# Kernel optimization log

Hardware: AMD Instinct MI355X
Metric: run time of the kernel (lower is better)

## Reference

```python
import jax, jax.numpy as jnp
import numpy as np

B, S, D, H, HD, R = 1, 3072, 2048, 16, 128, 16
ALPHA = 16.0
EPS = 1e-6


def _rope_freqs():
    # standard RoPE angles, interleave-duplicated so freqs[..., 0::2] gives the
    # per-pair cos values exactly as the torch module slices them
    inv = 1.0 / (10000.0 ** (np.arange(0, HD, 2, dtype=np.float32) / HD))  # [HD/2]
    ang = np.arange(S, dtype=np.float32)[:, None] * inv[None, :]           # [S, HD/2]
    cos = np.repeat(np.cos(ang), 2, axis=-1).reshape(1, S, 1, HD)
    sin = np.repeat(np.sin(ang), 2, axis=-1).reshape(1, S, 1, HD)
    return jnp.asarray(cos), jnp.asarray(sin)


def setup_inputs() -> dict:
    key = jax.random.key(0)
    ks = jax.random.split(key, 18)
    n = jax.random.normal
    WS = 0.02  # weight init scale
    freqs_cos, freqs_sin = _rope_freqs()
    return {
        "hidden_states": n(ks[0], (B, S, D), jnp.float32),
        "wq": n(ks[1], (D, D), jnp.float32) * WS,
        "bq": n(ks[2], (D,), jnp.float32) * WS,
        "wk": n(ks[3], (D, D), jnp.float32) * WS,
        "bk": n(ks[4], (D,), jnp.float32) * WS,
        "wv": n(ks[5], (D, D), jnp.float32) * WS,
        "bv": n(ks[6], (D,), jnp.float32) * WS,
        "wo": n(ks[7], (D, D), jnp.float32) * WS,
        "bo": n(ks[8], (D,), jnp.float32) * WS,
        "lq_down": n(ks[9], (R, D), jnp.float32) / R,
        "lq_up": n(ks[10], (D, R), jnp.float32) * WS,
        "lk_down": n(ks[11], (R, D), jnp.float32) / R,
        "lk_up": n(ks[12], (D, R), jnp.float32) * WS,
        "lv_down": n(ks[13], (R, D), jnp.float32) / R,
        "lv_up": n(ks[14], (D, R), jnp.float32) * WS,
        "lo_down": n(ks[15], (R, D), jnp.float32) / R,
        "lo_up": n(ks[16], (D, R), jnp.float32) * WS,
        "norm_q_w": jnp.ones((D,), jnp.float32),
        "norm_k_w": jnp.ones((D,), jnp.float32),
        "freqs_cos": freqs_cos,
        "freqs_sin": freqs_sin,
    }


def _lora(x, w_down, w_up, scale):
    return (x @ w_down.T) @ w_up.T * scale


def _rmsnorm(x, w):
    return x * jax.lax.rsqrt(jnp.mean(x * x, axis=-1, keepdims=True) + EPS) * w


def _apply_rotary(x, freqs_cos, freqs_sin):
    # x: [B,S,H,HD]; freqs: [1,S,1,HD]
    x1, x2 = x[..., 0::2], x[..., 1::2]
    c = freqs_cos[..., 0::2]
    s = freqs_sin[..., 1::2]
    even = x1 * c - x2 * s
    odd = x1 * s + x2 * c
    return jnp.stack([even, odd], axis=-1).reshape(x.shape)


def reference(hidden_states, wq, bq, wk, bk, wv, bv, wo, bo,
              lq_down, lq_up, lk_down, lk_up, lv_down, lv_up, lo_down, lo_up,
              norm_q_w, norm_k_w, freqs_cos, freqs_sin):
    scale = ALPHA / R
    x = hidden_states
    # qkv projections + LoRA adds (self-attention: encoder_hidden_states = hidden_states)
    q = x @ wq.T + bq + _lora(x, lq_down, lq_up, scale)
    k = x @ wk.T + bk + _lora(x, lk_down, lk_up, scale)
    v = x @ wv.T + bv + _lora(x, lv_down, lv_up, scale)
    # RMSNorm over full d_model, then split heads
    q = _rmsnorm(q, norm_q_w).reshape(B, S, H, HD)
    k = _rmsnorm(k, norm_k_w).reshape(B, S, H, HD)
    v = v.reshape(B, S, H, HD)
    # custom strided rotary embedding
    q = _apply_rotary(q, freqs_cos, freqs_sin)
    k = _apply_rotary(k, freqs_cos, freqs_sin)
    # SDPA (non-causal, no mask)
    scores = jnp.einsum('bihd,bjhd->bhij', q, k) / jnp.sqrt(jnp.float32(HD))
    attn = jax.nn.softmax(scores, axis=-1)
    o = jnp.einsum('bhij,bjhd->bihd', attn, v).reshape(B, S, D)
    # output projection + LoRA
    out = o @ wo.T + bo + _lora(o, lo_down, lo_up, scale)
    return out
```

## Files before the change

### kernel.cpp

```cpp
#include <hip/hip_runtime.h>
#include <stdint.h>

#define S_LEN 3072
#define DIM   2048
#define NH    16
#define HDIM  128
#define RANK  16
#define EPS_F 1e-6f
#define LORA_SCALE 1.0f
#define QK_SCALE 0.08838834764831845f
#define SM_MAX 24.0f

typedef unsigned short u16;
typedef __attribute__((ext_vector_type(8))) short short8;
typedef __attribute__((ext_vector_type(4))) float f32x4;
typedef __attribute__((ext_vector_type(16))) float f32x16;
typedef __attribute__((ext_vector_type(4))) unsigned short u16x4;
typedef __attribute__((ext_vector_type(8))) unsigned short u16x8;
typedef __attribute__((ext_vector_type(2))) unsigned short u16x2;
typedef __attribute__((ext_vector_type(4))) float float4a;
typedef __attribute__((ext_vector_type(4))) unsigned int uint4a;

__device__ __forceinline__ u16 f2b(float f) {
  uint32_t u = __builtin_bit_cast(uint32_t, f);
  u += 0x7fffu + ((u >> 16) & 1u);
  return (u16)(u >> 16);
}
__device__ __forceinline__ float b2f(u16 b) {
  uint32_t u = ((uint32_t)b) << 16;
  return __builtin_bit_cast(float, u);
}

__device__ __forceinline__ unsigned cvt_pk_bf16(float lo, float hi) {
  unsigned r;
  asm("v_cvt_pk_bf16_f32 %0, %1, %2" : "=v"(r) : "v"(lo), "v"(hi));
  return r;
}
__device__ __forceinline__ void pl32_swap(unsigned& a, unsigned& b) {
  asm("v_permlane32_swap_b32 %0, %1" : "+v"(a), "+v"(b));
}

__device__ __forceinline__ void g2l16(const void* g, void* l) {
  __builtin_amdgcn_global_load_lds(
      (__attribute__((address_space(1))) unsigned int*)g,
      (__attribute__((address_space(3))) unsigned int*)l, 16, 0, 0);
}

__global__ __launch_bounds__(256) void convf2b(const float* __restrict__ in,
                                               u16* __restrict__ out) {
  int i = (blockIdx.x * 256 + threadIdx.x) * 4;
  float4a v = *(const float4a*)(in + i);
  u16x4 o = { f2b(v[0]), f2b(v[1]), f2b(v[2]), f2b(v[3]) };
  *(u16x4*)(out + i) = o;
}

__global__ __launch_bounds__(256) void fold_lora4(
    const float* __restrict__ w0, const float* __restrict__ w1,
    const float* __restrict__ w2, const float* __restrict__ w3,
    const float* __restrict__ u0, const float* __restrict__ u1,
    const float* __restrict__ u2, const float* __restrict__ u3,
    const float* __restrict__ d0, const float* __restrict__ d1,
    const float* __restrict__ d2, const float* __restrict__ d3,
    u16* __restrict__ out_qkv, u16* __restrict__ out_o) {
  const int z = blockIdx.z;
  const float* W  = (z == 0) ? w0 : (z == 1) ? w1 : (z == 2) ? w2 : w3;
  const float* lu = (z == 0) ? u0 : (z == 1) ? u1 : (z == 2) ? u2 : u3;
  const float* ld = (z == 0) ? d0 : (z == 1) ? d1 : (z == 2) ? d2 : d3;
  u16* out = (z < 3) ? out_qkv + (size_t)z * DIM * DIM : out_o;
  __shared__ float lds_ld[16][136];
  __shared__ float lds_lu[64][17];
  const int tid = threadIdx.x;
  const int k0 = blockIdx.x * 128, n0 = blockIdx.y * 64;
  {
    int idx = tid * 8, r = idx >> 7, c = idx & 127;
    const float* src = ld + r * DIM + k0 + c;
#pragma unroll
    for (int e = 0; e < 8; ++e) lds_ld[r][c + e] = src[e];
  }
  {
    int idx = tid * 4, n = idx >> 4, r4 = idx & 15;
    const float* src = lu + (size_t)(n0 + n) * RANK + r4;
#pragma unroll
    for (int e = 0; e < 4; ++e) lds_lu[n][r4 + e] = src[e];
  }
  __syncthreads();
  const int n = tid >> 2;
  const int kg = (tid & 3) * 32;
  float luv[RANK];
#pragma unroll
  for (int r = 0; r < RANK; ++r) luv[r] = lds_lu[n][r];
  const float* wrow = W + (size_t)(n0 + n) * DIM + k0 + kg;
  u16* orow = out + (size_t)(n0 + n) * DIM + k0 + kg;
#pragma unroll
  for (int j = 0; j < 8; ++j) {
    float4a acc = *(const float4a*)(wrow + j * 4);
#pragma unroll
    for (int r = 0; r < RANK; ++r) {
      float4a lv = *(const float4a*)&lds_ld[r][kg + j * 4];
      acc += LORA_SCALE * luv[r] * lv;
    }
    u16x4 o = { f2b(acc[0]), f2b(acc[1]), f2b(acc[2]), f2b(acc[3]) };
    *(u16x4*)(orow + j * 4) = o;
  }
}

__global__ __launch_bounds__(256, 3) void gemm_fused(
    const u16* __restrict__ A, const u16* __restrict__ B,
    const float* __restrict__ b0, const float* __restrict__ b1,
    const float* __restrict__ b2, u16* __restrict__ c0, u16* __restrict__ c1,
    u16* __restrict__ c2t, float* __restrict__ Cf) {
  __shared__ __attribute__((aligned(16))) u16 As[128 * 64];
  __shared__ __attribute__((aligned(16))) u16 Bs[128 * 64];
  const int tid = threadIdx.x;
  const int wave = tid >> 6, lane = tid & 63;
  const int quad = lane >> 4, l15 = lane & 15;
  int nwg = gridDim.x * gridDim.y;
  int flat = blockIdx.y * gridDim.x + blockIdx.x;
  int cpx = nwg >> 3;
  int swz = (flat & 7) * cpx + (flat >> 3);
  const int m0 = (swz % gridDim.x) * 128;
  const int n0 = (swz / gridDim.x) * 128;
  const int mat = n0 >> 11;
  const float* bias = (mat == 0) ? b0 : (mat == 1 ? b1 : b2);
  u16* Cb = (mat == 0) ? c0 : c1;
  const int wr = wave >> 1, wc = wave & 1;
  f32x4 acc[4][4] = {};
  for (int kt = 0; kt < DIM / 64; ++kt) {
    __syncthreads();
#pragma unroll
    for (int i = 0; i < 4; ++i) {
      int chunk = i * 256 + wave * 64 + lane;
      int row = chunk >> 3, c8 = chunk & 7;
      g2l16(A + (size_t)(m0 + row) * DIM + kt * 64 + c8 * 8,
            As + (i * 256 + wave * 64) * 8);
      g2l16(B + (size_t)(n0 + row) * DIM + kt * 64 + c8 * 8,
            Bs + (i * 256 + wave * 64) * 8);
    }
    __syncthreads();
#pragma unroll
    for (int kc = 0; kc < 2; ++kc) {
      short8 af[4], bf[4];
#pragma unroll
      for (int tm = 0; tm < 4; ++tm)
        af[tm] = *(const short8*)(As + (wr * 64 + tm * 16 + l15) * 64 +
                                  kc * 32 + quad * 8);
#pragma unroll
      for (int tn = 0; tn < 4; ++tn)
        bf[tn] = *(const short8*)(Bs + (wc * 64 + tn * 16 + l15) * 64 +
                                  kc * 32 + quad * 8);
#pragma unroll
      for (int tm = 0; tm < 4; ++tm)
#pragma unroll
        for (int tn = 0; tn < 4; ++tn)
          acc[tm][tn] = __builtin_amdgcn_mfma_f32_16x16x32_bf16(
              af[tm], bf[tn], acc[tm][tn], 0, 0, 0);
    }
  }
#pragma unroll
  for (int tn = 0; tn < 4; ++tn) {
    int col = n0 + wc * 64 + tn * 16 + l15;
    int colL = col & (DIM - 1);
    float bcol = bias[colL];
#pragma unroll
    for (int tm = 0; tm < 4; ++tm) {
      int row0 = m0 + wr * 64 + tm * 16 + quad * 4;
      if (Cf) {
#pragma unroll
        for (int r = 0; r < 4; ++r)
          Cf[(size_t)(row0 + r) * DIM + colL] = acc[tm][tn][r] + bcol;
      } else if (mat == 2) {
        u16x4 o = { f2b(acc[tm][tn][0] + bcol), f2b(acc[tm][tn][1] + bcol),
                    f2b(acc[tm][tn][2] + bcol), f2b(acc[tm][tn][3] + bcol) };
        *(u16x4*)(c2t + (size_t)colL * S_LEN + row0) = o;
      } else {
#pragma unroll
        for (int r = 0; r < 4; ++r)
          Cb[(size_t)(row0 + r) * DIM + colL] = f2b(acc[tm][tn][r] + bcol);
      }
    }
  }
}

__global__ __launch_bounds__(256) void rms_rope(
    u16* __restrict__ q, u16* __restrict__ k,
    const float* __restrict__ nqw, const float* __restrict__ nkw,
    const float* __restrict__ fc, const float* __restrict__ fs) {
  const int s = blockIdx.x, tid = threadIdx.x;
  const int wave = tid >> 6, lane = tid & 63;
  float qv[8], kv[8];
  float sq = 0.f, sk = 0.f;
#pragma unroll
  for (int i = 0; i < 4; ++i) {
    int p = i * 256 + tid;
    u16x2 qa = *(const u16x2*)(q + (size_t)s * DIM + 2 * p);
    u16x2 ka = *(const u16x2*)(k + (size_t)s * DIM + 2 * p);
    qv[2 * i] = b2f(qa[0]); qv[2 * i + 1] = b2f(qa[1]);
    kv[2 * i] = b2f(ka[0]); kv[2 * i + 1] = b2f(ka[1]);
    sq += qv[2 * i] * qv[2 * i] + qv[2 * i + 1] * qv[2 * i + 1];
    sk += kv[2 * i] * kv[2 * i] + kv[2 * i + 1] * kv[2 * i + 1];
  }
#pragma unroll
  for (int off = 32; off > 0; off >>= 1) {
    sq += __shfl_down(sq, off);
    sk += __shfl_down(sk, off);
  }
  __shared__ float part[2][4];
  if (lane == 0) { part[0][wave] = sq; part[1][wave] = sk; }
  __syncthreads();
  float sumq = part[0][0] + part[0][1] + part[0][2] + part[0][3];
  float sumk = part[1][0] + part[1][1] + part[1][2] + part[1][3];
  float rq = rsqrtf(sumq * (1.f / DIM) + EPS_F);
  float rk = rsqrtf(sumk * (1.f / DIM) + EPS_F);
#pragma unroll
  for (int i = 0; i < 4; ++i) {
    int p = i * 256 + tid;
    int ip = p & 63;
    float c = fc[s * HDIM + 2 * ip];
    float sn = fs[s * HDIM + 2 * ip + 1];
    float e = qv[2 * i] * rq * nqw[2 * p];
    float o = qv[2 * i + 1] * rq * nqw[2 * p + 1];
    u16x2 qo = { f2b((e * c - o * sn) * QK_SCALE),
                 f2b((e * sn + o * c) * QK_SCALE) };
    *(u16x2*)(q + (size_t)s * DIM + 2 * p) = qo;
    float e2 = kv[2 * i] * rk * nkw[2 * p];
    float o2 = kv[2 * i + 1] * rk * nkw[2 * p + 1];
    u16x2 ko = { f2b(e2 * c - o2 * sn), f2b(e2 * sn + o2 * c) };
    *(u16x2*)(k + (size_t)s * DIM + 2 * p) = ko;
  }
}

__global__ __launch_bounds__(128, 2) void flash_attn(
    const u16* __restrict__ qb, const u16* __restrict__ kb,
    const u16* __restrict__ vt, u16* __restrict__ ob) {
  __shared__ __attribute__((aligned(16))) u16 Ks[64 * 128];
  __shared__ __attribute__((aligned(16))) u16 Vt[128 * 64];
  const int tid = threadIdx.x;
  const int wave = tid >> 6, lane = tid & 63;
  const int l31 = lane & 31, hi = lane >> 5;
  const int q0 = blockIdx.x * 64, h = blockIdx.y;
  short8 qf[8];
  {
    const u16* qrow =
        qb + (size_t)(q0 + wave * 32 + l31) * DIM + h * HDIM + hi * 8;
#pragma unroll
    for (int kc = 0; kc < 8; ++kc) qf[kc] = *(const short8*)(qrow + kc * 16);
  }
  f32x16 of[4] = {};
  float sP = 0.f;
  for (int it = 0; it < S_LEN / 64; ++it) {
    const int j0 = it * 64;
    __syncthreads();
#pragma unroll
    for (int i = 0; i < 8; ++i) {
      int slot = i * 128 + tid;
      {
        int j = slot >> 4, csp = slot & 15;
        int cg = csp ^ (j & 7);
        g2l16(kb + (size_t)(j0 + j) * DIM + h * HDIM + cg * 8,
              Ks + (i * 128 + wave * 64) * 8);
      }
      {
        int d = slot >> 3, cbp = slot & 7;
        int cbg = cbp ^ (d & 7);
        g2l16(vt + (size_t)(h * HDIM + d) * S_LEN + j0 + cbg * 8,
              Vt + (i * 128 + wave * 64) * 8);
      }
    }
    __syncthreads();
    f32x16 sf[2] = {};
    __builtin_amdgcn_s_setprio(1);
#pragma unroll
    for (int kc = 0; kc < 8; ++kc) {
      int gc = kc * 2 + hi;
#pragma unroll
      for (int mt = 0; mt < 2; ++mt) {
        int j = mt * 32 + l31;
        short8 kf = *(const short8*)(Ks + j * 128 + (gc ^ (j & 7)) * 8);
        sf[mt] =
            __builtin_amdgcn_mfma_f32_32x32x16_bf16(kf, qf[kc], sf[mt], 0, 0, 0);
      }
    }
    __builtin_amdgcn_s_setprio(0);
    short8 pb[4];
#pragma unroll
    for (int mt = 0; mt < 2; ++mt) {
      float p[16];
#pragma unroll
      for (int r = 0; r < 16; ++r) p[r] = __expf(sf[mt][r] - SM_MAX);
      float t0 = (p[0] + p[1]) + (p[2] + p[3]);
      float t1 = (p[4] + p[5]) + (p[6] + p[7]);
      float t2 = (p[8] + p[9]) + (p[10] + p[11]);
      float t3 = (p[12] + p[13]) + (p[14] + p[15]);
      sP += (t0 + t1) + (t2 + t3);
      unsigned w[8];
#pragma unroll
      for (int g = 0; g < 8; ++g) w[g] = cvt_pk_bf16(p[2 * g], p[2 * g + 1]);
      pl32_swap(w[0], w[2]);
      pl32_swap(w[1], w[3]);
      pl32_swap(w[4], w[6]);
      pl32_swap(w[5], w[7]);
      uint4a fe = { w[0], w[1], w[2], w[3] };
      uint4a fo = { w[4], w[5], w[6], w[7] };
      pb[2 * mt] = __builtin_bit_cast(short8, fe);
      pb[2 * mt + 1] = __builtin_bit_cast(short8, fo);
    }
    __builtin_amdgcn_s_setprio(1);
#pragma unroll
    for (int kc = 0; kc < 4; ++kc) {
      int gj = kc * 2 + hi;
#pragma unroll
      for (int mt2 = 0; mt2 < 4; ++mt2) {
        int d = mt2 * 32 + l31;
        short8 vf = *(const short8*)(Vt + d * 64 + (gj ^ (d & 7)) * 8);
        of[mt2] =
            __builtin_amdgcn_mfma_f32_32x32x16_bf16(vf, pb[kc], of[mt2], 0, 0, 0);
      }
    }
    __builtin_amdgcn_s_setprio(0);
  }
  float inv = 1.f / (sP + __shfl_xor(sP, 32));
  const int q = q0 + wave * 32 + l31;
#pragma unroll
  for (int mt2 = 0; mt2 < 4; ++mt2) {
#pragma unroll
    for (int t = 0; t < 4; ++t) {
      u16x4 o = { f2b(of[mt2][4 * t + 0] * inv), f2b(of[mt2][4 * t + 1] * inv),
                  f2b(of[mt2][4 * t + 2] * inv), f2b(of[mt2][4 * t + 3] * inv) };
      *(u16x4*)(ob + (size_t)q * DIM + h * HDIM + mt2 * 32 + t * 8 + hi * 4) = o;
    }
  }
}

extern "C" void kernel_launch(void* const* d_in, const int* in_sizes, int n_in,
                              void* d_out, int out_size, void* d_ws,
                              size_t ws_size, hipStream_t stream) {
  (void)in_sizes; (void)n_in; (void)out_size; (void)ws_size;
  const float* x   = (const float*)d_in[0];
  const float* wq  = (const float*)d_in[1];
  const float* bq  = (const float*)d_in[2];
  const float* wk  = (const float*)d_in[3];
  const float* bk  = (const float*)d_in[4];
  const float* wv  = (const float*)d_in[5];
  const float* bv  = (const float*)d_in[6];
  const float* wo  = (const float*)d_in[7];
  const float* bo  = (const float*)d_in[8];
  const float* lqd = (const float*)d_in[9];
  const float* lqu = (const float*)d_in[10];
  const float* lkd = (const float*)d_in[11];
  const float* lku = (const float*)d_in[12];
  const float* lvd = (const float*)d_in[13];
  const float* lvu = (const float*)d_in[14];
  const float* lod = (const float*)d_in[15];
  const float* lou = (const float*)d_in[16];
  const float* nqw = (const float*)d_in[17];
  const float* nkw = (const float*)d_in[18];
  const float* fc  = (const float*)d_in[19];
  const float* fs  = (const float*)d_in[20];

  char* ws = (char*)d_ws;
  size_t off = 0;
  auto alloc = [&](size_t bytes) {
    void* p = ws + off;
    off += (bytes + 255) & ~(size_t)255;
    return p;
  };
  const size_t SD2 = (size_t)S_LEN * DIM * 2;
  const size_t WW  = (size_t)DIM * DIM;
  u16* xb    = (u16*)alloc(SD2);
  u16* wqkvb = (u16*)alloc(3 * WW * 2);
  u16* wob   = (u16*)alloc(WW * 2);
  u16* q16   = (u16*)alloc(SD2);
  u16* k16   = (u16*)alloc(SD2);
  u16* vbT   = (u16*)alloc(SD2);
  u16* ob    = (u16*)alloc(SD2);

  convf2b<<<S_LEN * DIM / 1024, 256, 0, stream>>>(x, xb);
  fold_lora4<<<dim3(DIM / 128, DIM / 64, 4), 256, 0, stream>>>(
      wq, wk, wv, wo, lqu, lku, lvu, lou, lqd, lkd, lvd, lod, wqkvb, wob);
  gemm_fused<<<dim3(S_LEN / 128, 3 * DIM / 128), 256, 0, stream>>>(
      xb, wqkvb, bq, bk, bv, q16, k16, vbT, nullptr);
  rms_rope<<<S_LEN, 256, 0, stream>>>(q16, k16, nqw, nkw, fc, fs);
  flash_attn<<<dim3(S_LEN / 64, NH), 128, 0, stream>>>(q16, k16, vbT, ob);
  gemm_fused<<<dim3(S_LEN / 128, DIM / 128), 256, 0, stream>>>(
      ob, wob, bo, nullptr, nullptr, nullptr, nullptr, nullptr, (float*)d_out);
}
```

Before: 470.9 us.

## Split attention KV range across two blocks and combine partials in a new kernel

Flash attention now splits the key/value sequence in two along a third grid dimension and shrinks the KV tile from 64 to 32 rows. Each half writes unnormalized fp32 partial outputs and row sums, and a new combine kernel adds them, normalizes and converts to bf16. The goal is to double the block count (768 to 1536) for better CU occupancy on a 256-CU part, with smaller LDS tiles and the min-blocks launch bound removed. In exchange it adds about 50MB of fp32 partial traffic, an extra launch, and fewer MFMAs per barrier. It also rewrites exp as exp2 with an fma.

```diff
diff --git a/kernel.cpp b/kernel.cpp
--- a/kernel.cpp
+++ b/kernel.cpp
@@ -10,6 +10,8 @@
 #define LORA_SCALE 1.0f
 #define QK_SCALE 0.08838834764831845f
 #define SM_MAX 24.0f
+#define L2E 1.4426950408889634f
+#define KVSPLIT 2
 
 typedef unsigned short u16;
 typedef __attribute__((ext_vector_type(8))) short short8;
@@ -229,15 +231,18 @@
   }
 }
 
-__global__ __launch_bounds__(128, 2) void flash_attn(
+__global__ __launch_bounds__(128) void flash_attn(
     const u16* __restrict__ qb, const u16* __restrict__ kb,
-    const u16* __restrict__ vt, u16* __restrict__ ob) {
-  __shared__ __attribute__((aligned(16))) u16 Ks[64 * 128];
-  __shared__ __attribute__((aligned(16))) u16 Vt[128 * 64];
+    const u16* __restrict__ vt, float* __restrict__ opart,
+    float* __restrict__ spart) {
+  __shared__ __attribute__((aligned(16))) u16 Ks[32 * 128];
+  __shared__ __attribute__((aligned(16))) u16 Vt[128 * 32];
   const int tid = threadIdx.x;
   const int wave = tid >> 6, lane = tid & 63;
   const int l31 = lane & 31, hi = lane >> 5;
-  const int q0 = blockIdx.x * 64, h = blockIdx.y;
+  const int q0 = blockIdx.x * 64, h = blockIdx.y, kvh = blockIdx.z;
+  float* op = opart + (size_t)kvh * S_LEN * DIM;
+  float* sp = spart + (size_t)kvh * S_LEN * NH;
   short8 qf[8];
   {
     const u16* qrow =
@@ -247,11 +252,11 @@
   }
   f32x16 of[4] = {};
   float sP = 0.f;
-  for (int it = 0; it < S_LEN / 64; ++it) {
-    const int j0 = it * 64;
+  for (int it = 0; it < S_LEN / (32 * KVSPLIT); ++it) {
+    const int j0 = (kvh * (S_LEN / (32 * KVSPLIT)) + it) * 32;
     __syncthreads();
 #pragma unroll
-    for (int i = 0; i < 8; ++i) {
+    for (int i = 0; i < 4; ++i) {
       int slot = i * 128 + tid;
       {
         int j = slot >> 4, csp = slot & 15;
@@ -260,33 +265,28 @@
               Ks + (i * 128 + wave * 64) * 8);
       }
       {
-        int d = slot >> 3, cbp = slot & 7;
-        int cbg = cbp ^ (d & 7);
+        int d = slot >> 2, cbp = slot & 3;
+        int cbg = cbp ^ (d & 3);
         g2l16(vt + (size_t)(h * HDIM + d) * S_LEN + j0 + cbg * 8,
               Vt + (i * 128 + wave * 64) * 8);
       }
     }
     __syncthreads();
-    f32x16 sf[2] = {};
+    f32x16 sf = {};
     __builtin_amdgcn_s_setprio(1);
 #pragma unroll
     for (int kc = 0; kc < 8; ++kc) {
       int gc = kc * 2 + hi;
-#pragma unroll
-      for (int mt = 0; mt < 2; ++mt) {
-        int j = mt * 32 + l31;
-        short8 kf = *(const short8*)(Ks + j * 128 + (gc ^ (j & 7)) * 8);
-        sf[mt] =
-            __builtin_amdgcn_mfma_f32_32x32x16_bf16(kf, qf[kc], sf[mt], 0, 0, 0);
-      }
+      short8 kf = *(const short8*)(Ks + l31 * 128 + (gc ^ (l31 & 7)) * 8);
+      sf = __builtin_amdgcn_mfma_f32_32x32x16_bf16(kf, qf[kc], sf, 0, 0, 0);
     }
     __builtin_amdgcn_s_setprio(0);
-    short8 pb[4];
-#pragma unroll
-    for (int mt = 0; mt < 2; ++mt) {
+    short8 pb[2];
+    {
       float p[16];
 #pragma unroll
-      for (int r = 0; r < 16; ++r) p[r] = __expf(sf[mt][r] - SM_MAX);
+      for (int r = 0; r < 16; ++r)
+        p[r] = exp2f(fmaf(sf[r], L2E, -SM_MAX * L2E));
       float t0 = (p[0] + p[1]) + (p[2] + p[3]);
       float t1 = (p[4] + p[5]) + (p[6] + p[7]);
       float t2 = (p[8] + p[9]) + (p[10] + p[11]);
@@ -301,34 +301,52 @@
       pl32_swap(w[5], w[7]);
       uint4a fe = { w[0], w[1], w[2], w[3] };
       uint4a fo = { w[4], w[5], w[6], w[7] };
-      pb[2 * mt] = __builtin_bit_cast(short8, fe);
-      pb[2 * mt + 1] = __builtin_bit_cast(short8, fo);
+      pb[0] = __builtin_bit_cast(short8, fe);
+      pb[1] = __builtin_bit_cast(short8, fo);
     }
     __builtin_amdgcn_s_setprio(1);
 #pragma unroll
-    for (int kc = 0; kc < 4; ++kc) {
+    for (int kc = 0; kc < 2; ++kc) {
       int gj = kc * 2 + hi;
 #pragma unroll
       for (int mt2 = 0; mt2 < 4; ++mt2) {
         int d = mt2 * 32 + l31;
-        short8 vf = *(const short8*)(Vt + d * 64 + (gj ^ (d & 7)) * 8);
+        short8 vf = *(const short8*)(Vt + d * 32 + (gj ^ (d & 3)) * 8);
         of[mt2] =
             __builtin_amdgcn_mfma_f32_32x32x16_bf16(vf, pb[kc], of[mt2], 0, 0, 0);
       }
     }
     __builtin_amdgcn_s_setprio(0);
   }
-  float inv = 1.f / (sP + __shfl_xor(sP, 32));
   const int q = q0 + wave * 32 + l31;
+  float s = sP + __shfl_xor(sP, 32);
+  if (lane < 32) sp[(size_t)q * NH + h] = s;
 #pragma unroll
   for (int mt2 = 0; mt2 < 4; ++mt2) {
 #pragma unroll
     for (int t = 0; t < 4; ++t) {
-      u16x4 o = { f2b(of[mt2][4 * t + 0] * inv), f2b(of[mt2][4 * t + 1] * inv),
-                  f2b(of[mt2][4 * t + 2] * inv), f2b(of[mt2][4 * t + 3] * inv) };
-      *(u16x4*)(ob + (size_t)q * DIM + h * HDIM + mt2 * 32 + t * 8 + hi * 4) = o;
-    }
-  }
+      float4a o = { of[mt2][4 * t + 0], of[mt2][4 * t + 1],
+                    of[mt2][4 * t + 2], of[mt2][4 * t + 3] };
+      *(float4a*)(op + (size_t)q * DIM + h * HDIM + mt2 * 32 + t * 8 +
+                  hi * 4) = o;
+    }
+  }
+}
+
+__global__ __launch_bounds__(256) void comb(const float* __restrict__ o0,
+                                            const float* __restrict__ o1,
+                                            const float* __restrict__ s0,
+                                            const float* __restrict__ s1,
+                                            u16* __restrict__ ob) {
+  size_t i = ((size_t)blockIdx.x * 256 + threadIdx.x) * 4;
+  int q = (int)(i >> 11);
+  int h = (int)((i >> 7) & (NH - 1));
+  float inv = 1.f / (s0[(size_t)q * NH + h] + s1[(size_t)q * NH + h]);
+  float4a a = *(const float4a*)(o0 + i);
+  float4a b = *(const float4a*)(o1 + i);
+  u16x4 o = { f2b((a[0] + b[0]) * inv), f2b((a[1] + b[1]) * inv),
+              f2b((a[2] + b[2]) * inv), f2b((a[3] + b[3]) * inv) };
+  *(u16x4*)(ob + i) = o;
 }
 
 extern "C" void kernel_launch(void* const* d_in, const int* in_sizes, int n_in,
@@ -365,6 +383,7 @@
     return p;
   };
   const size_t SD2 = (size_t)S_LEN * DIM * 2;
+  const size_t SD4 = (size_t)S_LEN * DIM * 4;
   const size_t WW  = (size_t)DIM * DIM;
   u16* xb    = (u16*)alloc(SD2);
   u16* wqkvb = (u16*)alloc(3 * WW * 2);
@@ -373,6 +392,8 @@
   u16* k16   = (u16*)alloc(SD2);
   u16* vbT   = (u16*)alloc(SD2);
   u16* ob    = (u16*)alloc(SD2);
+  float* opart = (float*)alloc(KVSPLIT * SD4);
+  float* spart = (float*)alloc(KVSPLIT * S_LEN * NH * 4);
 
   convf2b<<<S_LEN * DIM / 1024, 256, 0, stream>>>(x, xb);
   fold_lora4<<<dim3(DIM / 128, DIM / 64, 4), 256, 0, stream>>>(
@@ -380,7 +401,11 @@
   gemm_fused<<<dim3(S_LEN / 128, 3 * DIM / 128), 256, 0, stream>>>(
       xb, wqkvb, bq, bk, bv, q16, k16, vbT, nullptr);
   rms_rope<<<S_LEN, 256, 0, stream>>>(q16, k16, nqw, nkw, fc, fs);
-  flash_attn<<<dim3(S_LEN / 64, NH), 128, 0, stream>>>(q16, k16, vbT, ob);
+  flash_attn<<<dim3(S_LEN / 64, NH, KVSPLIT), 128, 0, stream>>>(
+      q16, k16, vbT, opart, spart);
+  comb<<<S_LEN * DIM / 1024, 256, 0, stream>>>(
+      opart, opart + (size_t)S_LEN * DIM, spart, spart + (size_t)S_LEN * NH,
+      ob);
   gemm_fused<<<dim3(S_LEN / 128, DIM / 128), 256, 0, stream>>>(
       ob, wob, bo, nullptr, nullptr, nullptr, nullptr, nullptr, (float*)d_out);
 }
```

After: 517.3 us. 9.9% more time.
